# Performance work log

Measured on AMD Instinct MI355X. Metric: run time of the kernel, lower is better.

Reference implementation:

```python
import jax, jax.numpy as jnp
import numpy as np

GD, GH, GW = 8, 16, 16  # bilateral grid depth/height/width (fixed by pred.view(-1,12,8,16,16))


def _conv(x, w, b=None, stride=1, pad=1):
    y = jax.lax.conv_general_dilated(x, w, (stride, stride), ((pad, pad), (pad, pad)),
                                     dimension_numbers=('NCHW', 'OIHW', 'NCHW'))
    return y if b is None else y + b[None, :, None, None]


def _forward(high_res, low_res, ll1_w, ll1_b, ll2_w, ll2_b, ll3_w, ll3_b, ll4_w, ll4_b,
             lf1_w, lf1_b, lf2_w, gf1_w, gf1_b, gf2_w, gf2_b,
             fc1_w, fc1_b, fc2_w, fc2_b, fc3_w, fc3_b, pred_w, pred_b,
             pw_mat, pw_bias, pw_bias_tag, rho_a, rho_t):
    relu = jax.nn.relu
    bs, _, h, w = high_res.shape
    # ---- create_bilateral: low-res CNN -> bilateral grid (bs,12,8,16,16) ----
    x = relu(_conv(low_res, ll1_w, ll1_b, 2))
    x = relu(_conv(x, ll2_w, ll2_b, 2))
    x = relu(_conv(x, ll3_w, ll3_b, 2))
    x = relu(_conv(x, ll4_w, ll4_b, 2))            # (bs,64,16,16)
    lf = relu(_conv(x, lf1_w, lf1_b, 1))           # bn is Identity (use_bn=False)
    lf = _conv(lf, lf2_w, None, 1)                 # (bs,64,16,16)
    gf = relu(_conv(x, gf1_w, gf1_b, 2))
    gf = relu(_conv(gf, gf2_w, gf2_b, 2))          # (bs,64,4,4)
    gf = gf.reshape(bs, -1)                        # (bs,1024)
    gf = relu(gf @ fc1_w.T + fc1_b)
    gf = relu(gf @ fc2_w.T + fc2_b)
    gf = gf @ fc3_w.T + fc3_b                      # (bs,64)
    fusion = relu(gf[:, :, None, None] + lf)
    pred = _conv(fusion, pred_w, pred_b, 1, pad=0)  # 1x1 conv -> (bs,96,16,16)
    grid = pred.reshape(bs, 12, GD, GH, GW)
    # ---- create_guide: learned pointwise color curve (pw_guide=False path) ----
    g = jnp.einsum('ij,bjn->bin', pw_mat, high_res.reshape(bs, 3, h * w)) + pw_bias_tag  # (bs,3,N)
    t = relu(g[:, None, :, :] - rho_t[None, :, :, None])                                 # (bs,16,3,N)
    guide = jnp.einsum('bkcn,kc->bn', t, rho_a) + pw_bias                                # (bs,N)
    guide = guide.reshape(bs, h, w)
    # ---- slice_and_assemble_exp: trilinear grid slicing + per-pixel affine ----
    gx = (jnp.arange(w, dtype=jnp.float32) + 0.5) / w * GW     # (w,)
    gy = (jnp.arange(h, dtype=jnp.float32) + 0.5) / h * GH     # (h,)
    gz = jnp.clip(guide, 0.0, 1.0) * GD                        # (bs,h,w)
    fxf = jnp.maximum(jnp.floor(gx - 0.5), 0.0)
    fyf = jnp.maximum(jnp.floor(gy - 0.5), 0.0)
    fzf = jnp.maximum(jnp.floor(gz - 0.5), 0.0)
    wx = (gx - 0.5 - fxf)[None, None, None, :]                 # (1,1,1,w)  (torch keeps sign)
    wy = (gy - 0.5 - fyf)[None, None, :, None]                 # (1,1,h,1)
    wz = jnp.abs(gz - 0.5 - fzf)[:, None, :, :]                # (bs,1,h,w) (torch uses abs here)
    fx = fxf.astype(jnp.int32); cx = jnp.minimum(fx + 1, GW - 1)
    fy = fyf.astype(jnp.int32); cy = jnp.minimum(fy + 1, GH - 1)
    fz = fzf.astype(jnp.int32); cz = jnp.minimum(fz + 1, GD - 1)
    grid_flat = grid.reshape(bs, 12, GD * GH * GW)

    def gather(zi, yi, xi):
        # grid indexed as grid[b, c, z, y, x]
        lin = zi * (GH * GW) + yi[None, :, None] * GW + xi[None, None, :]   # (bs,h,w)
        out = jnp.take_along_axis(grid_flat, lin.reshape(bs, 1, h * w), axis=2)
        return out.reshape(bs, 12, h, w)

    a = (gather(fz, fy, fx) * (1 - wx) * (1 - wy) * (1 - wz)
         + gather(cz, fy, fx) * (1 - wx) * (1 - wy) * wz
         + gather(fz, cy, fx) * (1 - wx) * wy * (1 - wz)
         + gather(cz, cy, fx) * (1 - wx) * wy * wz
         + gather(fz, fy, cx) * wx * (1 - wy) * (1 - wz)
         + gather(cz, fy, cx) * wx * (1 - wy) * wz
         + gather(fz, cy, cx) * wx * wy * (1 - wz)
         + gather(cz, cy, cx) * wx * wy * wz)                  # (bs,12,h,w)
    a = a.reshape(bs, 3, 4, h, w)                              # 3 output channels x (3 affine + 1 bias)
    out = jnp.sum(a[:, :, :3] * high_res[:, None], axis=2) + a[:, :, 3]   # (bs,3,h,w)
    return out


def setup_inputs() -> dict:
    key = jax.random.key(0)
    ks = jax.random.split(key, 20)
    def W(k, shape, s=0.05):
        return jax.random.normal(k, shape, jnp.float32) * s
    z = lambda n: jnp.zeros((n,), jnp.float32)
    return {
        'high_res': jax.random.uniform(ks[0], (2, 3, 1024, 1024), jnp.float32),
        'low_res': jax.random.uniform(ks[1], (2, 3, 256, 256), jnp.float32),
        'll1_w': W(ks[2], (8, 3, 3, 3)), 'll1_b': z(8),
        'll2_w': W(ks[3], (16, 8, 3, 3)), 'll2_b': z(16),
        'll3_w': W(ks[4], (32, 16, 3, 3)), 'll3_b': z(32),
        'll4_w': W(ks[5], (64, 32, 3, 3)), 'll4_b': z(64),
        'lf1_w': W(ks[6], (64, 64, 3, 3)), 'lf1_b': z(64),
        'lf2_w': W(ks[7], (64, 64, 3, 3)),
        'gf1_w': W(ks[8], (64, 64, 3, 3)), 'gf1_b': z(64),
        'gf2_w': W(ks[9], (64, 64, 3, 3)), 'gf2_b': z(64),
        'fc1_w': W(ks[10], (256, 1024)), 'fc1_b': z(256),
        'fc2_w': W(ks[11], (128, 256)), 'fc2_b': z(128),
        'fc3_w': W(ks[12], (64, 128)), 'fc3_b': z(64),
        'pred_w': W(ks[13], (96, 64, 1, 1)), 'pred_b': z(96),
        'pw_mat': jnp.eye(3, dtype=jnp.float32) + jax.random.normal(ks[14], (1,), jnp.float32) * 1e-4,
        'pw_bias': jnp.eye(1, dtype=jnp.float32),
        'pw_bias_tag': jnp.zeros((3, 1), jnp.float32),
        'rho_a': jnp.ones((16, 3), jnp.float32),
        'rho_t': jax.random.uniform(ks[15], (16, 3), jnp.float32),
    }


def reference(high_res, low_res, ll1_w, ll1_b, ll2_w, ll2_b, ll3_w, ll3_b, ll4_w, ll4_b,
              lf1_w, lf1_b, lf2_w, gf1_w, gf1_b, gf2_w, gf2_b,
              fc1_w, fc1_b, fc2_w, fc2_b, fc3_w, fc3_b, pred_w, pred_b,
              pw_mat, pw_bias, pw_bias_tag, rho_a, rho_t):
    return _forward(high_res, low_res, ll1_w, ll1_b, ll2_w, ll2_b, ll3_w, ll3_b, ll4_w, ll4_b,
                    lf1_w, lf1_b, lf2_w, gf1_w, gf1_b, gf2_w, gf2_b,
                    fc1_w, fc1_b, fc2_w, fc2_b, fc3_w, fc3_b, pred_w, pred_b,
                    pw_mat, pw_bias, pw_bias_tag, rho_a, rho_t)
```

## Files before the change

kernel.cpp:

```cpp
#include <hip/hip_runtime.h>

#define BS 2
#define HR 1024
#define WR 1024

static inline int cdiv(int a, int b) { return (a + b - 1) / b; }

__device__ __forceinline__ void repack_body(int idx,
        const float* s0, const float* s1, const float* s2, const float* s3,
        const float* s4, const float* s5, const float* s6,
        float* d0, float* d1, float* d2, float* d3, float* d4, float* d5, float* d6,
        const float* fcs, float* fcd) {
    const int CONV_TOTAL = 171648;
    if (idx < CONV_TOTAL) {
        const float* src[7] = {s0, s1, s2, s3, s4, s5, s6};
        float* dst[7]       = {d0, d1, d2, d3, d4, d5, d6};
        const int cout[7] = {16, 32, 64, 64, 64, 64, 64};
        const int cin[7]  = {8, 16, 32, 64, 64, 64, 64};
        const int sz[7]   = {1152, 4608, 18432, 36864, 36864, 36864, 36864};
        int l = 0, e = idx;
        while (e >= sz[l]) { e -= sz[l]; ++l; }
        int Cin = cin[l], Cout = cout[l];
        int oc = e / (Cin * 9);
        int rem = e - oc * Cin * 9;
        int ic = rem / 9;
        int k  = rem - ic * 9;
        dst[l][((size_t)(k * Cout + oc)) * Cin + ic] = src[l][e];
    } else {
        int e = idx - CONV_TOTAL;
        if (e >= 262144) return;
        int o = e >> 10, j = e & 1023;
        int s = j >> 6, c = j & 63;
        fcd[e] = fcs[(o << 10) + (c << 4) + s];
    }
}

__device__ __forceinline__ void ll1_body(int idx, const float* in, const float* w,
                                         const float* bias, float* out) {
    if (idx >= BS * 128 * 128) return;
    int ox = idx & 127;
    int oy = (idx >> 7) & 127;
    int b  = idx >> 14;

    float acc[8];
#pragma unroll
    for (int oc = 0; oc < 8; ++oc) acc[oc] = bias[oc];
#pragma unroll
    for (int ky = 0; ky < 3; ++ky) {
        int iy = 2 * oy - 1 + ky;
        if (iy < 0 || iy >= 256) continue;
#pragma unroll
        for (int kx = 0; kx < 3; ++kx) {
            int ix = 2 * ox - 1 + kx;
            if (ix < 0 || ix >= 256) continue;
#pragma unroll
            for (int ic = 0; ic < 3; ++ic) {
                float v = in[(((size_t)b * 3 + ic) * 256 + iy) * 256 + ix];
#pragma unroll
                for (int oc = 0; oc < 8; ++oc)
                    acc[oc] += w[oc * 27 + ic * 9 + ky * 3 + kx] * v;
            }
        }
    }
    float* op = out + (size_t)idx * 8;
#pragma unroll
    for (int oc = 0; oc < 8; ++oc) op[oc] = fmaxf(acc[oc], 0.0f);
}

__global__ void k1_repack_ll1(
        const float* s0, const float* s1, const float* s2, const float* s3,
        const float* s4, const float* s5, const float* s6,
        float* d0, float* d1, float* d2, float* d3, float* d4, float* d5, float* d6,
        const float* fcs, float* fcd,
        const float* lr, const float* ll1w, const float* ll1b, float* b1out) {
    int bid = blockIdx.x;
    if (bid < 1695)
        repack_body(bid * 256 + threadIdx.x, s0, s1, s2, s3, s4, s5, s6,
                    d0, d1, d2, d3, d4, d5, d6, fcs, fcd);
    else
        ll1_body((bid - 1695) * 256 + threadIdx.x, lr, ll1w, ll1b, b1out);
}

template <int COUT, int CIN, int G, bool RELU, bool HASBIAS>
__device__ __forceinline__ void conv_body(int idx, const float* in, const float* wT,
                                          const float* bias, float* out,
                                          int Hin, int Win, int Hout, int Wout, int stride) {
    constexpr int ICPG = CIN / G;
    int total = BS * Hout * Wout * COUT * G;
    if (idx >= total) return;
    int icg = idx & (G - 1);
    int oc  = (idx / G) & (COUT - 1);
    int pix = idx / (G * COUT);
    int ox = pix % Wout;
    int oy = (pix / Wout) % Hout;
    int b  = pix / (Wout * Hout);

    int iy0 = oy * stride - 1;
    int ix0 = ox * stride - 1;
    float acc = 0.0f;
#pragma unroll
    for (int ky = 0; ky < 3; ++ky) {
        int iy = iy0 + ky;
        if (iy < 0 || iy >= Hin) continue;
#pragma unroll
        for (int kx = 0; kx < 3; ++kx) {
            int ix = ix0 + kx;
            if (ix < 0 || ix >= Win) continue;
            int k = ky * 3 + kx;
            const float* wp = wT + ((size_t)(k * COUT + oc)) * CIN + icg * ICPG;
            const float* ip = in + ((size_t)((b * Hin + iy) * Win + ix)) * CIN + icg * ICPG;
#pragma unroll
            for (int ic4 = 0; ic4 < ICPG / 4; ++ic4) {
                float4 wv = *reinterpret_cast<const float4*>(wp + ic4 * 4);
                float4 iv = *reinterpret_cast<const float4*>(ip + ic4 * 4);
                acc += wv.x * iv.x + wv.y * iv.y + wv.z * iv.z + wv.w * iv.w;
            }
        }
    }
    if (G > 1) {
#pragma unroll
        for (int off = G / 2; off > 0; off >>= 1) acc += __shfl_xor(acc, off, 64);
    }
    if (icg == 0) {
        if (HASBIAS) acc += bias[oc];
        if (RELU) acc = fmaxf(acc, 0.0f);
        out[(size_t)pix * COUT + oc] = acc;
    }
}

template <int COUT, int CIN, int G, bool RELU, bool HASBIAS>
__global__ void conv_nhwc_split(const float* __restrict__ in, const float* __restrict__ wT,
                                const float* __restrict__ bias, float* __restrict__ out,
                                int Hin, int Win, int Hout, int Wout, int stride) {
    conv_body<COUT, CIN, G, RELU, HASBIAS>(blockIdx.x * blockDim.x + threadIdx.x,
                                           in, wT, bias, out, Hin, Win, Hout, Wout, stride);
}

__global__ void k5_lf1_gf1(const float* __restrict__ b4,
                           const float* __restrict__ wlf1T, const float* __restrict__ lf1b,
                           float* __restrict__ lf1o,
                           const float* __restrict__ wgf1T, const float* __restrict__ gf1b,
                           float* __restrict__ gf1o) {
    int bid = blockIdx.x;
    if (bid < 1024)
        conv_body<64, 64, 8, true, true>(bid * 256 + threadIdx.x, b4, wlf1T, lf1b, lf1o, 16, 16, 16, 16, 1);
    else
        conv_body<64, 64, 8, true, true>((bid - 1024) * 256 + threadIdx.x, b4, wgf1T, gf1b, gf1o, 16, 16, 8, 8, 2);
}

__global__ void k6_lf2_gf2(const float* __restrict__ lf1o,
                           const float* __restrict__ wlf2T, float* __restrict__ lf2o,
                           const float* __restrict__ gf1o,
                           const float* __restrict__ wgf2T, const float* __restrict__ gf2b,
                           float* __restrict__ gf2o) {
    int bid = blockIdx.x;
    if (bid < 1024)
        conv_body<64, 64, 8, false, false>(bid * 256 + threadIdx.x, lf1o, wlf2T, nullptr, lf2o, 16, 16, 16, 16, 1);
    else
        conv_body<64, 64, 8, true, true>((bid - 1024) * 256 + threadIdx.x, gf1o, wgf2T, gf2b, gf2o, 8, 8, 4, 4, 2);
}

__global__ void fc_wave_kernel(const float* __restrict__ in, const float* __restrict__ w,
                               const float* __restrict__ bias, float* __restrict__ out,
                               int In, int Out, int do_relu) {
    int wid  = (blockIdx.x * blockDim.x + threadIdx.x) >> 6;
    int lane = threadIdx.x & 63;
    if (wid >= BS * Out) return;
    int o = wid % Out;
    int b = wid / Out;
    const float* ip = in + (size_t)b * In;
    const float* wp = w + (size_t)o * In;

    float acc = 0.0f;
    for (int i = lane * 4; i < In; i += 64 * 4) {
        float4 wv = *reinterpret_cast<const float4*>(wp + i);
        float4 iv = *reinterpret_cast<const float4*>(ip + i);
        acc += wv.x * iv.x + wv.y * iv.y + wv.z * iv.z + wv.w * iv.w;
    }
#pragma unroll
    for (int off = 32; off > 0; off >>= 1) acc += __shfl_xor(acc, off, 64);
    if (lane == 0) {
        acc += bias[o];
        if (do_relu) acc = fmaxf(acc, 0.0f);
        out[(size_t)b * Out + o] = acc;
    }
}

__global__ void __launch_bounds__(1024) fc23_kernel(
        const float* __restrict__ fc1o,
        const float* __restrict__ fc2w, const float* __restrict__ fc2b,
        const float* __restrict__ fc3w, const float* __restrict__ fc3b,
        float* __restrict__ fc3o) {
    __shared__ float s_fc2[128];
    int b = blockIdx.x, tid = threadIdx.x;

    {
        int o = tid >> 3, p = tid & 7;
        const float* wp = fc2w + (size_t)o * 256 + p * 32;
        const float* ip = fc1o + (size_t)b * 256 + p * 32;
        float acc = 0.0f;
#pragma unroll
        for (int i = 0; i < 8; ++i) {
            float4 wv = *reinterpret_cast<const float4*>(wp + i * 4);
            float4 iv = *reinterpret_cast<const float4*>(ip + i * 4);
            acc += wv.x * iv.x + wv.y * iv.y + wv.z * iv.z + wv.w * iv.w;
        }
        acc += __shfl_xor(acc, 1, 64);
        acc += __shfl_xor(acc, 2, 64);
        acc += __shfl_xor(acc, 4, 64);
        if (p == 0) s_fc2[o] = fmaxf(acc + fc2b[o], 0.0f);
    }
    __syncthreads();

    {
        int o = tid >> 4, p = tid & 15;
        const float* wp = fc3w + (size_t)o * 128 + p * 8;
        const float* ip = s_fc2 + p * 8;
        float acc = 0.0f;
#pragma unroll
        for (int i = 0; i < 2; ++i) {
            float4 wv = *reinterpret_cast<const float4*>(wp + i * 4);
            float4 iv = *reinterpret_cast<const float4*>(ip + i * 4);
            acc += wv.x * iv.x + wv.y * iv.y + wv.z * iv.z + wv.w * iv.w;
        }
        acc += __shfl_xor(acc, 1, 64);
        acc += __shfl_xor(acc, 2, 64);
        acc += __shfl_xor(acc, 4, 64);
        acc += __shfl_xor(acc, 8, 64);
        if (p == 0) fc3o[(size_t)b * 64 + o] = acc + fc3b[o];
    }
}

__global__ void fuse_pred_kernel(const float* __restrict__ lf, const float* __restrict__ gfv,
                                 const float* __restrict__ pw, const float* __restrict__ pb,
                                 float* __restrict__ gt) {
    int idx  = blockIdx.x * blockDim.x + threadIdx.x;
    int gid  = idx >> 4;
    int lane = idx & 15;
    int total = BS * 96 * 256;
    if (gid >= total) return;
    int sp = gid % 256;
    int oc = (gid / 256) % 96;
    int b  = gid / (256 * 96);

    float4 lv = *reinterpret_cast<const float4*>(lf + ((size_t)(b * 256 + sp) * 64) + lane * 4);
    float4 gv = *reinterpret_cast<const float4*>(gfv + (size_t)b * 64 + lane * 4);
    float4 wv = *reinterpret_cast<const float4*>(pw + (size_t)oc * 64 + lane * 4);
    float fx0 = fmaxf(gv.x + lv.x, 0.0f);
    float fx1 = fmaxf(gv.y + lv.y, 0.0f);
    float fx2 = fmaxf(gv.z + lv.z, 0.0f);
    float fx3 = fmaxf(gv.w + lv.w, 0.0f);
    float acc = wv.x * fx0 + wv.y * fx1 + wv.z * fx2 + wv.w * fx3;
#pragma unroll
    for (int off = 8; off > 0; off >>= 1) acc += __shfl_xor(acc, off, 64);
    if (lane == 0) {
        int z = oc & 7, c12 = oc >> 3;
        int y = sp >> 4, x = sp & 15;
        gt[((size_t)b * 2048 + (size_t)(z * 16 + y) * 16 + x) * 12 + c12] = acc + pb[oc];
    }
}

__global__ void slice_row_kernel(const float* __restrict__ hr, const float* __restrict__ gt,
                                 const float* __restrict__ pw_mat, const float* __restrict__ pw_bias,
                                 const float* __restrict__ pw_bias_tag,
                                 const float* __restrict__ rho_a, const float* __restrict__ rho_t,
                                 float* __restrict__ out) {
    __shared__ float slab[1536];
    int t = threadIdx.x;
    int y = blockIdx.x & (HR - 1);
    int b = blockIdx.x >> 10;

    float gyv = (y + 0.5f) * (16.0f / HR);
    float fyf = fmaxf(floorf(gyv - 0.5f), 0.0f);
    float wyv = gyv - 0.5f - fyf;
    int fy = (int)fyf; int cy = min(fy + 1, 15);
    float ey = 1.0f - wyv;

    const float* gb = gt + (size_t)b * 24576;
    for (int i = t; i < 384; i += 256) {
        int s = i * 4;
        int zz = s / 192;
        int rc = s - zz * 192;
        float4 vf = *reinterpret_cast<const float4*>(gb + (size_t)(zz * 16 + fy) * 192 + rc);
        float4 vc = *reinterpret_cast<const float4*>(gb + (size_t)(zz * 16 + cy) * 192 + rc);
        float4 v;
        v.x = ey * vf.x + wyv * vc.x;
        v.y = ey * vf.y + wyv * vc.y;
        v.z = ey * vf.z + wyv * vc.z;
        v.w = ey * vf.w + wyv * vc.w;
        *reinterpret_cast<float4*>(slab + s) = v;
    }
    __syncthreads();

    const size_t plane = (size_t)HR * WR;
    int x0 = t * 4;
    const float* hp = hr + (size_t)b * 3 * plane + (size_t)y * WR + x0;
    float4 R4 = *reinterpret_cast<const float4*>(hp);
    float4 G4 = *reinterpret_cast<const float4*>(hp + plane);
    float4 B4 = *reinterpret_cast<const float4*>(hp + 2 * plane);
    float rr[4] = {R4.x, R4.y, R4.z, R4.w};
    float gg[4] = {G4.x, G4.y, G4.z, G4.w};
    float bb[4] = {B4.x, B4.y, B4.z, B4.w};

    float m0 = pw_mat[0], m1 = pw_mat[1], m2 = pw_mat[2];
    float m3 = pw_mat[3], m4 = pw_mat[4], m5 = pw_mat[5];
    float m6 = pw_mat[6], m7 = pw_mat[7], m8 = pw_mat[8];
    float bt0 = pw_bias_tag[0], bt1 = pw_bias_tag[1], bt2 = pw_bias_tag[2];
    float pb = pw_bias[0];

    float g0[4], g1[4], g2[4], guide[4];
#pragma unroll
    for (int j = 0; j < 4; ++j) {
        g0[j] = m0 * rr[j] + m1 * gg[j] + m2 * bb[j] + bt0;
        g1[j] = m3 * rr[j] + m4 * gg[j] + m5 * bb[j] + bt1;
        g2[j] = m6 * rr[j] + m7 * gg[j] + m8 * bb[j] + bt2;
        guide[j] = pb;
    }
#pragma unroll
    for (int k = 0; k < 16; ++k) {
        float t0 = rho_t[k * 3 + 0], t1 = rho_t[k * 3 + 1], t2 = rho_t[k * 3 + 2];
        float a0 = rho_a[k * 3 + 0], a1 = rho_a[k * 3 + 1], a2 = rho_a[k * 3 + 2];
#pragma unroll
        for (int j = 0; j < 4; ++j) {
            guide[j] += fmaxf(g0[j] - t0, 0.0f) * a0;
            guide[j] += fmaxf(g1[j] - t1, 0.0f) * a1;
            guide[j] += fmaxf(g2[j] - t2, 0.0f) * a2;
        }
    }

    float o0[4], o1[4], o2[4];
#pragma unroll
    for (int j = 0; j < 4; ++j) {
        int x = x0 + j;
        float r = rr[j], g = gg[j], bl = bb[j];

        float gx = (x + 0.5f) * (16.0f / WR);
        float gz = fminf(fmaxf(guide[j], 0.0f), 1.0f) * 8.0f;
        float fxf = fmaxf(floorf(gx - 0.5f), 0.0f);
        float fzf = fmaxf(floorf(gz - 0.5f), 0.0f);
        float wxv = gx - 0.5f - fxf;
        float wzv = fabsf(gz - 0.5f - fzf);
        int fx = (int)fxf; int cx = min(fx + 1, 15);
        int fz = (int)fzf; int cz = min(fz + 1, 7);
        float ex = 1.0f - wxv, ez = 1.0f - wzv;

        int o_f = fz * 192 + fx * 12;
        int o_c = cz * 192 + fx * 12;
        int dxo = (cx - fx) * 12;

        float w0 = ex * ez, w1 = ex * wzv, w2 = wxv * ez, w3 = wxv * wzv;

        float4 a0 = {0,0,0,0}, a1 = {0,0,0,0}, a2 = {0,0,0,0};
        const int offs[4] = {o_f, o_c, o_f + dxo, o_c + dxo};
        const float wts[4] = {w0, w1, w2, w3};
#pragma unroll
        for (int c = 0; c < 4; ++c) {
            const float* p = slab + offs[c];
            float4 v0 = *reinterpret_cast<const float4*>(p);
            float4 v1 = *reinterpret_cast<const float4*>(p + 4);
            float4 v2 = *reinterpret_cast<const float4*>(p + 8);
            float wv = wts[c];
            a0.x += wv * v0.x; a0.y += wv * v0.y; a0.z += wv * v0.z; a0.w += wv * v0.w;
            a1.x += wv * v1.x; a1.y += wv * v1.y; a1.z += wv * v1.z; a1.w += wv * v1.w;
            a2.x += wv * v2.x; a2.y += wv * v2.y; a2.z += wv * v2.z; a2.w += wv * v2.w;
        }
        o0[j] = a0.x * r + a0.y * g + a0.z * bl + a0.w;
        o1[j] = a1.x * r + a1.y * g + a1.z * bl + a1.w;
        o2[j] = a2.x * r + a2.y * g + a2.z * bl + a2.w;
    }

    float* op = out + (size_t)b * 3 * plane + (size_t)y * WR + x0;
    *reinterpret_cast<float4*>(op)              = make_float4(o0[0], o0[1], o0[2], o0[3]);
    *reinterpret_cast<float4*>(op + plane)      = make_float4(o1[0], o1[1], o1[2], o1[3]);
    *reinterpret_cast<float4*>(op + 2 * plane)  = make_float4(o2[0], o2[1], o2[2], o2[3]);
}

extern "C" void kernel_launch(void* const* d_in, const int* in_sizes, int n_in,
                              void* d_out, int out_size, void* d_ws, size_t ws_size,
                              hipStream_t stream) {
    const float* high_res   = (const float*)d_in[0];
    const float* low_res    = (const float*)d_in[1];
    const float* ll1_w = (const float*)d_in[2];  const float* ll1_b = (const float*)d_in[3];
    const float* ll2_w = (const float*)d_in[4];  const float* ll2_b = (const float*)d_in[5];
    const float* ll3_w = (const float*)d_in[6];  const float* ll3_b = (const float*)d_in[7];
    const float* ll4_w = (const float*)d_in[8];  const float* ll4_b = (const float*)d_in[9];
    const float* lf1_w = (const float*)d_in[10]; const float* lf1_b = (const float*)d_in[11];
    const float* lf2_w = (const float*)d_in[12];
    const float* gf1_w = (const float*)d_in[13]; const float* gf1_b = (const float*)d_in[14];
    const float* gf2_w = (const float*)d_in[15]; const float* gf2_b = (const float*)d_in[16];
    const float* fc1_w = (const float*)d_in[17]; const float* fc1_b = (const float*)d_in[18];
    const float* fc2_w = (const float*)d_in[19]; const float* fc2_b = (const float*)d_in[20];
    const float* fc3_w = (const float*)d_in[21]; const float* fc3_b = (const float*)d_in[22];
    const float* pred_w = (const float*)d_in[23]; const float* pred_b = (const float*)d_in[24];
    const float* pw_mat = (const float*)d_in[25];
    const float* pw_bias = (const float*)d_in[26];
    const float* pw_bias_tag = (const float*)d_in[27];
    const float* rho_a = (const float*)d_in[28];
    const float* rho_t = (const float*)d_in[29];

    float* ws = (float*)d_ws;
    float* b1    = ws;
    float* b2    = b1 + 262144;
    float* b3    = b2 + 131072;
    float* b4    = b3 + 65536;
    float* lf1o  = b4 + 32768;
    float* lf2o  = lf1o + 32768;
    float* gf1o  = lf2o + 32768;
    float* gf2o  = gf1o + 8192;
    float* fc1o  = gf2o + 2048;
    float* fc3o  = fc1o + 512;
    float* gt    = fc3o + 128;
    float* wll2T = gt + 49152;
    float* wll3T = wll2T + 1152;
    float* wll4T = wll3T + 4608;
    float* wlf1T = wll4T + 18432;
    float* wlf2T = wlf1T + 36864;
    float* wgf1T = wlf2T + 36864;
    float* wgf2T = wgf1T + 36864;
    float* wfc1T = wgf2T + 36864;

    float* out = (float*)d_out;
    dim3 blk(256);

    k1_repack_ll1<<<1695 + 128, blk, 0, stream>>>(
        ll2_w, ll3_w, ll4_w, lf1_w, lf2_w, gf1_w, gf2_w,
        wll2T, wll3T, wll4T, wlf1T, wlf2T, wgf1T, wgf2T,
        fc1_w, wfc1T,
        low_res, ll1_w, ll1_b, b1);
    conv_nhwc_split<16, 8, 1, true, true><<<cdiv(BS*64*64*16, 256), blk, 0, stream>>>(b1, wll2T, ll2_b, b2, 128, 128, 64, 64, 2);
    conv_nhwc_split<32, 16, 1, true, true><<<cdiv(BS*32*32*32, 256), blk, 0, stream>>>(b2, wll3T, ll3_b, b3, 64, 64, 32, 32, 2);
    conv_nhwc_split<64, 32, 4, true, true><<<cdiv(BS*16*16*64*4, 256), blk, 0, stream>>>(b3, wll4T, ll4_b, b4, 32, 32, 16, 16, 2);
    k5_lf1_gf1<<<1024 + 256, blk, 0, stream>>>(b4, wlf1T, lf1_b, lf1o, wgf1T, gf1_b, gf1o);
    k6_lf2_gf2<<<1024 + 64, blk, 0, stream>>>(lf1o, wlf2T, lf2o, gf1o, wgf2T, gf2_b, gf2o);
    fc_wave_kernel<<<cdiv(BS*256*64, 256), blk, 0, stream>>>(gf2o, wfc1T, fc1_b, fc1o, 1024, 256, 1);
    fc23_kernel<<<BS, dim3(1024), 0, stream>>>(fc1o, fc2_w, fc2_b, fc3_w, fc3_b, fc3o);
    fuse_pred_kernel<<<cdiv(BS*96*256*16, 256), blk, 0, stream>>>(lf2o, fc3o, pred_w, pred_b, gt);
    slice_row_kernel<<<BS*HR, blk, 0, stream>>>(high_res, gt, pw_mat, pw_bias, pw_bias_tag,
                                                rho_a, rho_t, out);
}
```

Baseline: 78.47 us.

## Transpose FC1 weights via LDS and double input-channel split in conv kernels

The FC1 weight repack now uses one block per output row and stages the 1024-element row in shared memory, so both the reads and the writes are coalesced. This replaces the old strided gather. Every small conv layer also raises its input-channel group split G (1→2, 1→4, 4→8, 8→16), giving more threads per output to fill the GPU on these small layers. The cost is a larger cross-lane reduction and more threads doing less work each.

```diff
diff --git a/kernel.cpp b/kernel.cpp
--- a/kernel.cpp
+++ b/kernel.cpp
@@ -6,33 +6,25 @@
 
 static inline int cdiv(int a, int b) { return (a + b - 1) / b; }
 
-__device__ __forceinline__ void repack_body(int idx,
+__device__ __forceinline__ void repack_conv_body(int idx,
         const float* s0, const float* s1, const float* s2, const float* s3,
         const float* s4, const float* s5, const float* s6,
-        float* d0, float* d1, float* d2, float* d3, float* d4, float* d5, float* d6,
-        const float* fcs, float* fcd) {
+        float* d0, float* d1, float* d2, float* d3, float* d4, float* d5, float* d6) {
     const int CONV_TOTAL = 171648;
-    if (idx < CONV_TOTAL) {
-        const float* src[7] = {s0, s1, s2, s3, s4, s5, s6};
-        float* dst[7]       = {d0, d1, d2, d3, d4, d5, d6};
-        const int cout[7] = {16, 32, 64, 64, 64, 64, 64};
-        const int cin[7]  = {8, 16, 32, 64, 64, 64, 64};
-        const int sz[7]   = {1152, 4608, 18432, 36864, 36864, 36864, 36864};
-        int l = 0, e = idx;
-        while (e >= sz[l]) { e -= sz[l]; ++l; }
-        int Cin = cin[l], Cout = cout[l];
-        int oc = e / (Cin * 9);
-        int rem = e - oc * Cin * 9;
-        int ic = rem / 9;
-        int k  = rem - ic * 9;
-        dst[l][((size_t)(k * Cout + oc)) * Cin + ic] = src[l][e];
-    } else {
-        int e = idx - CONV_TOTAL;
-        if (e >= 262144) return;
-        int o = e >> 10, j = e & 1023;
-        int s = j >> 6, c = j & 63;
-        fcd[e] = fcs[(o << 10) + (c << 4) + s];
-    }
+    if (idx >= CONV_TOTAL) return;
+    const float* src[7] = {s0, s1, s2, s3, s4, s5, s6};
+    float* dst[7]       = {d0, d1, d2, d3, d4, d5, d6};
+    const int cout[7] = {16, 32, 64, 64, 64, 64, 64};
+    const int cin[7]  = {8, 16, 32, 64, 64, 64, 64};
+    const int sz[7]   = {1152, 4608, 18432, 36864, 36864, 36864, 36864};
+    int l = 0, e = idx;
+    while (e >= sz[l]) { e -= sz[l]; ++l; }
+    int Cin = cin[l], Cout = cout[l];
+    int oc = e / (Cin * 9);
+    int rem = e - oc * Cin * 9;
+    int ic = rem / 9;
+    int k  = rem - ic * 9;
+    dst[l][((size_t)(k * Cout + oc)) * Cin + ic] = src[l][e];
 }
 
 __device__ __forceinline__ void ll1_body(int idx, const float* in, const float* w,
@@ -74,11 +66,25 @@
         const float* fcs, float* fcd,
         const float* lr, const float* ll1w, const float* ll1b, float* b1out) {
     int bid = blockIdx.x;
-    if (bid < 1695)
-        repack_body(bid * 256 + threadIdx.x, s0, s1, s2, s3, s4, s5, s6,
-                    d0, d1, d2, d3, d4, d5, d6, fcs, fcd);
-    else
-        ll1_body((bid - 1695) * 256 + threadIdx.x, lr, ll1w, ll1b, b1out);
+    int t = threadIdx.x;
+    if (bid < 256) {
+        __shared__ float lds[1024];
+        int o = bid;
+#pragma unroll
+        for (int k = 0; k < 4; ++k)
+            lds[t + k * 256] = fcs[(o << 10) + t + k * 256];
+        __syncthreads();
+#pragma unroll
+        for (int k = 0; k < 4; ++k) {
+            int j = t + k * 256;
+            fcd[(o << 10) + j] = lds[(j & 63) * 16 + (j >> 6)];
+        }
+    } else if (bid < 927) {
+        repack_conv_body((bid - 256) * 256 + t, s0, s1, s2, s3, s4, s5, s6,
+                         d0, d1, d2, d3, d4, d5, d6);
+    } else {
+        ll1_body((bid - 927) * 256 + t, lr, ll1w, ll1b, b1out);
+    }
 }
 
 template <int COUT, int CIN, int G, bool RELU, bool HASBIAS>
@@ -142,10 +148,10 @@
                            const float* __restrict__ wgf1T, const float* __restrict__ gf1b,
                            float* __restrict__ gf1o) {
     int bid = blockIdx.x;
-    if (bid < 1024)
-        conv_body<64, 64, 8, true, true>(bid * 256 + threadIdx.x, b4, wlf1T, lf1b, lf1o, 16, 16, 16, 16, 1);
+    if (bid < 2048)
+        conv_body<64, 64, 16, true, true>(bid * 256 + threadIdx.x, b4, wlf1T, lf1b, lf1o, 16, 16, 16, 16, 1);
     else
-        conv_body<64, 64, 8, true, true>((bid - 1024) * 256 + threadIdx.x, b4, wgf1T, gf1b, gf1o, 16, 16, 8, 8, 2);
+        conv_body<64, 64, 16, true, true>((bid - 2048) * 256 + threadIdx.x, b4, wgf1T, gf1b, gf1o, 16, 16, 8, 8, 2);
 }
 
 __global__ void k6_lf2_gf2(const float* __restrict__ lf1o,
@@ -154,10 +160,10 @@
                            const float* __restrict__ wgf2T, const float* __restrict__ gf2b,
                            float* __restrict__ gf2o) {
     int bid = blockIdx.x;
-    if (bid < 1024)
-        conv_body<64, 64, 8, false, false>(bid * 256 + threadIdx.x, lf1o, wlf2T, nullptr, lf2o, 16, 16, 16, 16, 1);
+    if (bid < 2048)
+        conv_body<64, 64, 16, false, false>(bid * 256 + threadIdx.x, lf1o, wlf2T, nullptr, lf2o, 16, 16, 16, 16, 1);
     else
-        conv_body<64, 64, 8, true, true>((bid - 1024) * 256 + threadIdx.x, gf1o, wgf2T, gf2b, gf2o, 8, 8, 4, 4, 2);
+        conv_body<64, 64, 16, true, true>((bid - 2048) * 256 + threadIdx.x, gf1o, wgf2T, gf2b, gf2o, 8, 8, 4, 4, 2);
 }
 
 __global__ void fc_wave_kernel(const float* __restrict__ in, const float* __restrict__ w,
@@ -422,16 +428,16 @@
     float* out = (float*)d_out;
     dim3 blk(256);
 
-    k1_repack_ll1<<<1695 + 128, blk, 0, stream>>>(
+    k1_repack_ll1<<<1055, blk, 0, stream>>>(
         ll2_w, ll3_w, ll4_w, lf1_w, lf2_w, gf1_w, gf2_w,
         wll2T, wll3T, wll4T, wlf1T, wlf2T, wgf1T, wgf2T,
         fc1_w, wfc1T,
         low_res, ll1_w, ll1_b, b1);
-    conv_nhwc_split<16, 8, 1, true, true><<<cdiv(BS*64*64*16, 256), blk, 0, stream>>>(b1, wll2T, ll2_b, b2, 128, 128, 64, 64, 2);
-    conv_nhwc_split<32, 16, 1, true, true><<<cdiv(BS*32*32*32, 256), blk, 0, stream>>>(b2, wll3T, ll3_b, b3, 64, 64, 32, 32, 2);
-    conv_nhwc_split<64, 32, 4, true, true><<<cdiv(BS*16*16*64*4, 256), blk, 0, stream>>>(b3, wll4T, ll4_b, b4, 32, 32, 16, 16, 2);
-    k5_lf1_gf1<<<1024 + 256, blk, 0, stream>>>(b4, wlf1T, lf1_b, lf1o, wgf1T, gf1_b, gf1o);
-    k6_lf2_gf2<<<1024 + 64, blk, 0, stream>>>(lf1o, wlf2T, lf2o, gf1o, wgf2T, gf2_b, gf2o);
+    conv_nhwc_split<16, 8, 2, true, true><<<cdiv(BS*64*64*16*2, 256), blk, 0, stream>>>(b1, wll2T, ll2_b, b2, 128, 128, 64, 64, 2);
+    conv_nhwc_split<32, 16, 4, true, true><<<cdiv(BS*32*32*32*4, 256), blk, 0, stream>>>(b2, wll3T, ll3_b, b3, 64, 64, 32, 32, 2);
+    conv_nhwc_split<64, 32, 8, true, true><<<cdiv(BS*16*16*64*8, 256), blk, 0, stream>>>(b3, wll4T, ll4_b, b4, 32, 32, 16, 16, 2);
+    k5_lf1_gf1<<<2048 + 512, blk, 0, stream>>>(b4, wlf1T, lf1_b, lf1o, wgf1T, gf1_b, gf1o);
+    k6_lf2_gf2<<<2048 + 128, blk, 0, stream>>>(lf1o, wlf2T, lf2o, gf1o, wgf2T, gf2_b, gf2o);
     fc_wave_kernel<<<cdiv(BS*256*64, 256), blk, 0, stream>>>(gf2o, wfc1T, fc1_b, fc1o, 1024, 256, 1);
     fc23_kernel<<<BS, dim3(1024), 0, stream>>>(fc1o, fc2_w, fc2_b, fc3_w, fc3_b, fc3o);
     fuse_pred_kernel<<<cdiv(BS*96*256*16, 256), blk, 0, stream>>>(lf2o, fc3o, pred_w, pred_b, gt);
```

Result: no change. 77.98 us (-0.6%).
